# Optimization experiments

Hardware: AMD Instinct MI355X
Metric: run time of the kernel (lower is better)

The kernel has to match this reference:

```python
import jax, jax.numpy as jnp
import numpy as np

D_MODEL = 384
D_STATE = 16
D_CONV = 3
EXPAND = 2
D_INNER = EXPAND * D_MODEL          # 768
DT_RANK = (D_MODEL + 15) // 16      # 24 (mamba_ssm 'auto' rank = ceil(d_model/16))
B_, H_, W_ = 8, 32, 32


def setup_inputs() -> dict:
    key = jax.random.key(0)
    ks = jax.random.split(key, 8)
    s = lambda k, shape, scale: jax.random.normal(k, shape, jnp.float32) * scale
    x = jax.random.normal(ks[0], (B_, D_MODEL, H_, W_), jnp.float32)
    in_proj_w = s(ks[1], (2 * D_INNER, D_MODEL), 0.02)
    conv_w = s(ks[2], (D_INNER, D_CONV), 0.1)          # depthwise conv kernels
    conv_b = jnp.zeros((D_INNER,), jnp.float32)
    x_proj_w = s(ks[3], (DT_RANK + 2 * D_STATE, D_INNER), 0.02)
    dt_proj_w = s(ks[4], (D_INNER, DT_RANK), 0.1)
    # bias so that softplus(bias) ~= 0.01 (mamba dt init)
    dt_proj_b = jnp.log(jnp.expm1(jnp.full((D_INNER,), 0.01, jnp.float32)))
    # S4D-real init: A = -[1..N] per channel, stored as log
    A_log = jnp.log(jnp.broadcast_to(
        jnp.arange(1, D_STATE + 1, dtype=jnp.float32), (D_INNER, D_STATE)))
    D = jnp.ones((D_INNER,), jnp.float32)
    out_proj_w = s(ks[5], (D_MODEL, D_INNER), 0.02)
    return dict(x=x, in_proj_w=in_proj_w, conv_w=conv_w, conv_b=conv_b,
                x_proj_w=x_proj_w, dt_proj_w=dt_proj_w, dt_proj_b=dt_proj_b,
                A_log=A_log, D=D, out_proj_w=out_proj_w)


def _mamba(xseq, in_proj_w, conv_w, conv_b, x_proj_w,
           dt_proj_w, dt_proj_b, A_log, D, out_proj_w):
    # xseq: (B, L, d_model)
    B, L, _ = xseq.shape
    xz = xseq @ in_proj_w.T                         # (B, L, 2*d_inner)
    xin, z = jnp.split(xz, 2, axis=-1)

    # depthwise causal conv1d over L
    xc = jnp.transpose(xin, (0, 2, 1))              # (B, d_inner, L)
    xc = jnp.pad(xc, ((0, 0), (0, 0), (D_CONV - 1, 0)))
    xc = jax.lax.conv_general_dilated(
        xc, conv_w[:, None, :], (1,), 'VALID',
        dimension_numbers=('NCH', 'OIH', 'NCH'),
        feature_group_count=D_INNER)
    xc = xc + conv_b[None, :, None]
    u = jax.nn.silu(jnp.transpose(xc, (0, 2, 1)))   # (B, L, d_inner)

    dbc = u @ x_proj_w.T                            # (B, L, dt_rank + 2N)
    dt = dbc[..., :DT_RANK]
    Bm = dbc[..., DT_RANK:DT_RANK + D_STATE]        # (B, L, N)
    Cm = dbc[..., DT_RANK + D_STATE:]               # (B, L, N)
    dt = jax.nn.softplus(dt @ dt_proj_w.T + dt_proj_b)  # (B, L, d_inner)
    A = -jnp.exp(A_log)                             # (d_inner, N)

    def step(h, inp):
        dt_t, B_t, C_t, u_t = inp                   # (B,d), (B,N), (B,N), (B,d)
        dA = jnp.exp(dt_t[..., None] * A)           # (B, d_inner, N)
        h = dA * h + (dt_t * u_t)[..., None] * B_t[:, None, :]
        y = jnp.einsum('bdn,bn->bd', h, C_t)
        return h, y

    h0 = jnp.zeros((B, D_INNER, D_STATE), xseq.dtype)
    _, ys = jax.lax.scan(step, h0, (jnp.swapaxes(dt, 0, 1), jnp.swapaxes(Bm, 0, 1),
                                    jnp.swapaxes(Cm, 0, 1), jnp.swapaxes(u, 0, 1)))
    y = jnp.swapaxes(ys, 0, 1) + u * D              # (B, L, d_inner)
    y = y * jax.nn.silu(z)
    return y @ out_proj_w.T                         # (B, L, d_model)


def reference(x, in_proj_w, conv_w, conv_b, x_proj_w,
              dt_proj_w, dt_proj_b, A_log, D, out_proj_w):
    # x: (B, C, H, W) -> sequence (B, H*W, C) -> Mamba -> back to (B, C, H, W)
    B, C, H, W = x.shape
    xseq = jnp.transpose(x, (0, 2, 3, 1)).reshape(B, H * W, C)
    y = _mamba(xseq, in_proj_w, conv_w, conv_b, x_proj_w,
               dt_proj_w, dt_proj_b, A_log, D, out_proj_w)
    return jnp.transpose(y.reshape(B, H, W, C), (0, 3, 1, 2))
```

## Files before the change

kernel.cpp:

```cpp
#include <hip/hip_runtime.h>

#define D_MODEL 384
#define D_STATE 16
#define D_INNER 768
#define DT_RANK 24
#define NB 8
#define LSEQ 1024
#define NROWS (NB * LSEQ)
#define DBC_N 56
#define SEG 16
#define NSEG 64

typedef unsigned short u16;
typedef __attribute__((ext_vector_type(8))) short bf16x8;
typedef __attribute__((ext_vector_type(4))) float f32x4;
typedef __attribute__((ext_vector_type(16))) float f32x16;

__device__ __forceinline__ float silu(float x) { return x / (1.f + __expf(-x)); }

__device__ __forceinline__ u16 f2bf_rne(float v, float& hval) {
    unsigned u = __builtin_bit_cast(unsigned, v);
    unsigned h = (u + 0x7FFFu + ((u >> 16) & 1u)) >> 16;
    hval = __builtin_bit_cast(float, h << 16);
    return (u16)h;
}

__device__ __forceinline__ void split2(float v, u16& h, u16& l) {
    float hval, dummy;
    h = f2bf_rne(v, hval);
    l = f2bf_rne(v - hval, dummy);
}

template <int CTRL>
__device__ __forceinline__ float dpp_mov(float v) {
    return __builtin_bit_cast(float, __builtin_amdgcn_update_dpp(
        0, __builtin_bit_cast(int, v), CTRL, 0xf, 0xf, false));
}

__global__ __launch_bounds__(256) void k_splitw(const float* __restrict__ src,
                                                u16* __restrict__ hi, u16* __restrict__ lo,
                                                int count) {
    const int i = blockIdx.x * 256 + threadIdx.x;
    if (i >= count) return;
    u16 h, l;
    split2(src[i], h, l);
    hi[i] = h; lo[i] = l;
}

__global__ __launch_bounds__(256) void k_splitw_pad(const float* __restrict__ src,
                                                    u16* __restrict__ hi, u16* __restrict__ lo) {
    const int i = blockIdx.x * 256 + threadIdx.x;
    if (i >= 64 * 768) return;
    const int row = i / 768;
    u16 h = 0, l = 0;
    if (row < DBC_N) split2(src[i], h, l);
    hi[i] = h; lo[i] = l;
}

__global__ __launch_bounds__(256) void k_splitT(const float* __restrict__ src,
                                                u16* __restrict__ hi, u16* __restrict__ lo,
                                                int R) {
    __shared__ float s[32][33];
    const int r0 = blockIdx.x * 32, c0 = blockIdx.y * 32, b = blockIdx.z;
    const int t = threadIdx.x;
    const int cc = t & 31, rr = t >> 5;
#pragma unroll
    for (int p = 0; p < 4; ++p)
        s[rr + p * 8][cc] = src[((size_t)b * R + r0 + rr + p * 8) * LSEQ + c0 + cc];
    __syncthreads();
    const int rr2 = t & 31, cc2 = t >> 5;
#pragma unroll
    for (int p = 0; p < 4; ++p) {
        const int c = cc2 + p * 8;
        u16 h, l;
        split2(s[rr2][c], h, l);
        const size_t idx = ((size_t)b * LSEQ + c0 + c) * R + r0 + rr2;
        hi[idx] = h; lo[idx] = l;
    }
}

template <int K, int MODE>
__global__ __launch_bounds__(256) void k_gemm(const u16* __restrict__ Ahi,
                                              const u16* __restrict__ Alo,
                                              const u16* __restrict__ Bhi,
                                              const u16* __restrict__ Blo,
                                              float* __restrict__ out0,
                                              float* __restrict__ out1) {
    constexpr int KT = K / 32;
    __shared__ u16 lA[2][2][512 * 8];
    __shared__ u16 lB[2][2][512 * 8];
    const int tid = threadIdx.x;
    const int n0 = blockIdx.x * 128;
    const int m0 = blockIdx.y * 128;

    bf16x8 rah[2], ral[2], rbh[2], rbl[2];
    auto load_kt = [&](int kt) {
        const int ko = kt * 32;
#pragma unroll
        for (int i = 0; i < 2; ++i) {
            const int slot = tid + 256 * i;
            const size_t aoff = (size_t)(m0 + (slot & 127)) * K + ko + (slot >> 7) * 8;
            const size_t boff = (size_t)(n0 + (slot & 127)) * K + ko + (slot >> 7) * 8;
            rah[i] = *reinterpret_cast<const bf16x8*>(Ahi + aoff);
            ral[i] = *reinterpret_cast<const bf16x8*>(Alo + aoff);
            rbh[i] = *reinterpret_cast<const bf16x8*>(Bhi + boff);
            rbl[i] = *reinterpret_cast<const bf16x8*>(Blo + boff);
        }
    };
    auto write_kt = [&](int buf) {
#pragma unroll
        for (int i = 0; i < 2; ++i) {
            const int slot = tid + 256 * i;
            *reinterpret_cast<bf16x8*>(&lA[buf][0][slot * 8]) = rah[i];
            *reinterpret_cast<bf16x8*>(&lA[buf][1][slot * 8]) = ral[i];
            *reinterpret_cast<bf16x8*>(&lB[buf][0][slot * 8]) = rbh[i];
            *reinterpret_cast<bf16x8*>(&lB[buf][1][slot * 8]) = rbl[i];
        }
    };

    load_kt(0);
    write_kt(0);
    if (KT > 1) load_kt(1);

    const int lane = tid & 63, w = tid >> 6;
    const int wm = w >> 1, wn = w & 1;
    const int r32 = lane & 31, g2 = lane >> 5;

    f32x16 acc[2][2] = {};
    for (int kt = 0; kt < KT; ++kt) {
        const int cur = kt & 1;
        __syncthreads();
#pragma unroll
        for (int ks = 0; ks < 2; ++ks) {
            bf16x8 ah[2], al[2], bh[2], bl[2];
#pragma unroll
            for (int mi = 0; mi < 2; ++mi) {
                const int ai = ((ks * 2 + g2) * 128 + wm * 64 + mi * 32 + r32) * 8;
                ah[mi] = *reinterpret_cast<const bf16x8*>(&lA[cur][0][ai]);
                al[mi] = *reinterpret_cast<const bf16x8*>(&lA[cur][1][ai]);
            }
#pragma unroll
            for (int ni = 0; ni < 2; ++ni) {
                const int bi = ((ks * 2 + g2) * 128 + wn * 64 + ni * 32 + r32) * 8;
                bh[ni] = *reinterpret_cast<const bf16x8*>(&lB[cur][0][bi]);
                bl[ni] = *reinterpret_cast<const bf16x8*>(&lB[cur][1][bi]);
            }
#pragma unroll
            for (int mi = 0; mi < 2; ++mi)
#pragma unroll
                for (int ni = 0; ni < 2; ++ni) {
                    acc[mi][ni] = __builtin_amdgcn_mfma_f32_32x32x16_bf16(
                        ah[mi], bh[ni], acc[mi][ni], 0, 0, 0);
                    acc[mi][ni] = __builtin_amdgcn_mfma_f32_32x32x16_bf16(
                        ah[mi], bl[ni], acc[mi][ni], 0, 0, 0);
                    acc[mi][ni] = __builtin_amdgcn_mfma_f32_32x32x16_bf16(
                        al[mi], bh[ni], acc[mi][ni], 0, 0, 0);
                }
        }
        if (kt + 1 < KT) {
            __syncthreads();
            write_kt(cur ^ 1);
            if (kt + 2 < KT) load_kt(kt + 2);
        }
    }

    const int b_idx = m0 >> 10;
    const int l0b = m0 & 1023;
    if (MODE == 0) {
        if (n0 < D_INNER) {
#pragma unroll
            for (int mi = 0; mi < 2; ++mi) {
#pragma unroll
                for (int ni = 0; ni < 2; ++ni) {
                    const int n = n0 + wn * 64 + ni * 32 + r32;
#pragma unroll
                    for (int reg = 0; reg < 16; ++reg) {
                        const int m = m0 + wm * 64 + mi * 32 +
                                      (reg & 3) + 8 * (reg >> 2) + 4 * g2;
                        out0[(size_t)m * D_INNER + n] = acc[mi][ni][reg];
                    }
                }
            }
        } else {
#pragma unroll
            for (int mi = 0; mi < 2; ++mi) {
#pragma unroll
                for (int ni = 0; ni < 2; ++ni) {
                    const int d = (n0 - D_INNER) + wn * 64 + ni * 32 + r32;
#pragma unroll
                    for (int q = 0; q < 4; ++q) {
                        const int l = l0b + wm * 64 + mi * 32 + 8 * q + 4 * g2;
                        float4 v = make_float4(silu(acc[mi][ni][q * 4 + 0]),
                                               silu(acc[mi][ni][q * 4 + 1]),
                                               silu(acc[mi][ni][q * 4 + 2]),
                                               silu(acc[mi][ni][q * 4 + 3]));
                        *reinterpret_cast<float4*>(
                            &out1[((size_t)b_idx * D_INNER + d) * LSEQ + l]) = v;
                    }
                }
            }
        }
    } else {
#pragma unroll
        for (int mi = 0; mi < 2; ++mi) {
#pragma unroll
            for (int ni = 0; ni < 2; ++ni) {
                const int n = n0 + wn * 64 + ni * 32 + r32;
#pragma unroll
                for (int q = 0; q < 4; ++q) {
                    const int l = l0b + wm * 64 + mi * 32 + 8 * q + 4 * g2;
                    float4 v = make_float4(acc[mi][ni][q * 4 + 0], acc[mi][ni][q * 4 + 1],
                                           acc[mi][ni][q * 4 + 2], acc[mi][ni][q * 4 + 3]);
                    *reinterpret_cast<float4*>(
                        &out0[((size_t)b_idx * D_MODEL + n) * LSEQ + l]) = v;
                }
            }
        }
    }
}

__global__ __launch_bounds__(256) void k_xprojm(const u16* __restrict__ Uhi,
                                                const u16* __restrict__ Ulo,
                                                const u16* __restrict__ Whi,
                                                const u16* __restrict__ Wlo,
                                                float* __restrict__ dbc,
                                                float* __restrict__ bct) {
    __shared__ u16 lA[2][2][64 * 32];
    __shared__ u16 lB[2][2][64 * 32];
    const int tid = threadIdx.x;
    const int m0 = blockIdx.x * 64;
    const int arow = tid >> 2, acol = (tid & 3) * 8;

    bf16x8 rah, ral, rbh, rbl;
    auto load_kt = [&](int kt) {
        const int ko = kt * 32;
        const size_t aoff = (size_t)(m0 + arow) * D_INNER + ko + acol;
        const size_t boff = (size_t)arow * D_INNER + ko + acol;
        rah = *reinterpret_cast<const bf16x8*>(Uhi + aoff);
        ral = *reinterpret_cast<const bf16x8*>(Ulo + aoff);
        rbh = *reinterpret_cast<const bf16x8*>(Whi + boff);
        rbl = *reinterpret_cast<const bf16x8*>(Wlo + boff);
    };
    auto write_kt = [&](int buf) {
        *reinterpret_cast<bf16x8*>(&lA[buf][0][arow * 32 + acol]) = rah;
        *reinterpret_cast<bf16x8*>(&lA[buf][1][arow * 32 + acol]) = ral;
        *reinterpret_cast<bf16x8*>(&lB[buf][0][arow * 32 + acol]) = rbh;
        *reinterpret_cast<bf16x8*>(&lB[buf][1][arow * 32 + acol]) = rbl;
    };

    load_kt(0);
    write_kt(0);
    load_kt(1);

    const int lane = tid & 63, w = tid >> 6;
    const int fr = lane & 15, g = lane >> 4;
    f32x4 acc[4] = {};
    for (int kt = 0; kt < 24; ++kt) {
        const int cur = kt & 1;
        __syncthreads();
        const int af = (w * 16 + fr) * 32 + g * 8;
        bf16x8 ah = *reinterpret_cast<const bf16x8*>(&lA[cur][0][af]);
        bf16x8 al = *reinterpret_cast<const bf16x8*>(&lA[cur][1][af]);
        bf16x8 bh[4], bl[4];
#pragma unroll
        for (int ni = 0; ni < 4; ++ni) {
            const int bf = (ni * 16 + fr) * 32 + g * 8;
            bh[ni] = *reinterpret_cast<const bf16x8*>(&lB[cur][0][bf]);
            bl[ni] = *reinterpret_cast<const bf16x8*>(&lB[cur][1][bf]);
        }
#pragma unroll
        for (int ni = 0; ni < 4; ++ni) {
            acc[ni] = __builtin_amdgcn_mfma_f32_16x16x32_bf16(ah, bh[ni], acc[ni], 0, 0, 0);
            acc[ni] = __builtin_amdgcn_mfma_f32_16x16x32_bf16(ah, bl[ni], acc[ni], 0, 0, 0);
            acc[ni] = __builtin_amdgcn_mfma_f32_16x16x32_bf16(al, bh[ni], acc[ni], 0, 0, 0);
        }
        if (kt + 1 < 24) {
            __syncthreads();
            write_kt(cur ^ 1);
            if (kt + 2 < 24) load_kt(kt + 2);
        }
    }

    const int b_idx = m0 >> 10;
#pragma unroll
    for (int ni = 0; ni < 4; ++ni) {
        const int col = ni * 16 + fr;
#pragma unroll
        for (int j = 0; j < 4; ++j) {
            const int r = w * 16 + g * 4 + j;
            const float v = acc[ni][j];
            if (col < DT_RANK) {
                dbc[(size_t)(m0 + r) * DBC_N + col] = v;
            } else if (col < DBC_N) {
                bct[((size_t)b_idx * 32 + (col - DT_RANK)) * LSEQ + ((m0 & 1023) + r)] = v;
            }
        }
    }
}

__global__ __launch_bounds__(256) void k_conv(const float* __restrict__ xin,
                                              const float* __restrict__ cw,
                                              const float* __restrict__ cb,
                                              u16* __restrict__ u_hi,
                                              u16* __restrict__ u_lo,
                                              float* __restrict__ uT) {
    __shared__ float xs[34][32];
    __shared__ float us[32][33];
    const int d0 = blockIdx.x * 32;
    const int l0 = blockIdx.y * 32;
    const int b  = blockIdx.z;
    const int t = threadIdx.x;
    const int dd = t & 31, r = t >> 5;
    for (int rr = r; rr < 34; rr += 8) {
        const int l = l0 - 2 + rr;
        xs[rr][dd] = (l >= 0) ? xin[((size_t)b * LSEQ + l) * D_INNER + d0 + dd] : 0.f;
    }
    __syncthreads();
    const float w0 = cw[(d0 + dd) * 3 + 0], w1 = cw[(d0 + dd) * 3 + 1], w2 = cw[(d0 + dd) * 3 + 2];
    const float bv = cb[d0 + dd];
#pragma unroll
    for (int p = 0; p < 4; ++p) {
        const int li = r + p * 8;
        float acc = bv;
        acc = fmaf(xs[li + 0][dd], w0, acc);
        acc = fmaf(xs[li + 1][dd], w1, acc);
        acc = fmaf(xs[li + 2][dd], w2, acc);
        const float uv = silu(acc);
        u16 h, l;
        split2(uv, h, l);
        const size_t idx = ((size_t)b * LSEQ + l0 + li) * D_INNER + d0 + dd;
        u_hi[idx] = h; u_lo[idx] = l;
        us[li][dd] = uv;
    }
    __syncthreads();
    const int ll = t & 31, dg = t >> 5;
#pragma unroll
    for (int p = 0; p < 4; ++p) {
        const int dl = dg + p * 8;
        uT[((size_t)b * D_INNER + d0 + dl) * LSEQ + l0 + ll] = us[ll][dl];
    }
}

__global__ __launch_bounds__(256) void k_dtproj(const float* __restrict__ dbc,
                                                const float* __restrict__ W,
                                                const float* __restrict__ bias,
                                                float* __restrict__ dtT) {
    __shared__ float sd[64][25];
    __shared__ float sw[64][24];
    __shared__ float sb[64];
    const int d0 = blockIdx.x * 64;
    const int row0 = blockIdx.y * 64;
    const int b = row0 >> 10, lr0 = row0 & 1023;
    const int t = threadIdx.x;
    for (int e = t; e < 64 * 24; e += 256) {
        const int rl = e / 24, rr = e - rl * 24;
        sd[rl][rr] = dbc[(size_t)(row0 + rl) * DBC_N + rr];
        sw[rl][rr] = W[(size_t)(d0 + rl) * DT_RANK + rr];
    }
    if (t < 64) sb[t] = bias[d0 + t];
    __syncthreads();
    const int ll = t & 63, dg = t >> 6;
    for (int dd = 0; dd < 16; ++dd) {
        const int dl = dg * 16 + dd;
        float acc = sb[dl];
#pragma unroll
        for (int r = 0; r < DT_RANK; ++r) acc = fmaf(sd[ll][r], sw[dl][r], acc);
        const float v = (acc > 20.f) ? acc : log1pf(__expf(acc));
        dtT[((size_t)b * D_INNER + d0 + dl) * LSEQ + lr0 + ll] = v;
    }
}

__global__ __launch_bounds__(1024, 8) void k_scan(float* dtyT,
                                                  const float* __restrict__ uT,
                                                  const float* __restrict__ szT,
                                                  const float* __restrict__ bct,
                                                  const float* __restrict__ A_log,
                                                  const float* __restrict__ Dp) {
    __shared__ float dt_s[LSEQ], u_s[LSEQ], sz_s[LSEQ], y_s[LSEQ];
    __shared__ float Pb[16][NSEG + 2], Hb[16][NSEG + 2];
    const int t = threadIdx.x;
    const int d = blockIdx.x;
    const int b = blockIdx.y;
    const size_t base = ((size_t)b * D_INNER + d) * LSEQ;
    if (t < 256) {
        *reinterpret_cast<float4*>(&dt_s[t * 4]) =
            *reinterpret_cast<const float4*>(&dtyT[base + t * 4]);
    } else if (t < 512) {
        const int q = (t - 256) * 4;
        *reinterpret_cast<float4*>(&u_s[q]) = *reinterpret_cast<const float4*>(&uT[base + q]);
    } else if (t < 768) {
        const int q = (t - 512) * 4;
        *reinterpret_cast<float4*>(&sz_s[q]) = *reinterpret_cast<const float4*>(&szT[base + q]);
    }
    const int n = t & 15, seg = t >> 4;
    const float Aval2 = -__expf(A_log[d * D_STATE + n]) * 1.44269504088896f;
    const float Dv = Dp[d];
    float Breg[SEG];
    {
        const size_t bb = ((size_t)b * 32 + n) * LSEQ + seg * SEG;
#pragma unroll
        for (int q = 0; q < SEG; q += 4)
            *reinterpret_cast<float4*>(&Breg[q]) = *reinterpret_cast<const float4*>(&bct[bb + q]);
    }
    __syncthreads();
    const int l0 = seg * SEG;
    float h = 0.f, P = 1.f;
#pragma unroll
    for (int l = 0; l < SEG; ++l) {
        const float dtv = dt_s[l0 + l];
        const float a = exp2f(dtv * Aval2);
        const float x = dtv * u_s[l0 + l] * Breg[l];
        Breg[l] = x;
        h = fmaf(a, h, x);
        P *= a;
    }
    Pb[n][seg] = P;
    Hb[n][seg] = h;
    float Creg[SEG];
    {
        const size_t cc = ((size_t)b * 32 + 16 + n) * LSEQ + seg * SEG;
#pragma unroll
        for (int q = 0; q < SEG; q += 4)
            *reinterpret_cast<float4*>(&Creg[q]) = *reinterpret_cast<const float4*>(&bct[cc + q]);
    }
    __syncthreads();
    {
        const int w = t >> 6, lane = t & 63;
        float Pw = Pb[w][lane], Hw = Hb[w][lane];
#pragma unroll
        for (int off = 1; off < NSEG; off <<= 1) {
            const float Pp = __shfl_up(Pw, off);
            const float Hp = __shfl_up(Hw, off);
            if (lane >= off) {
                Hw = fmaf(Hp, Pw, Hw);
                Pw *= Pp;
            }
        }
        Hb[w][lane] = Hw;
    }
    __syncthreads();
    h = (seg == 0) ? 0.f : Hb[n][seg - 1];
#pragma unroll
    for (int l = 0; l < SEG; ++l) {
        const float a = exp2f(dt_s[l0 + l] * Aval2);
        h = fmaf(a, h, Breg[l]);
        float p = h * Creg[l];
        p += dpp_mov<0x128>(p);
        p += dpp_mov<0x124>(p);
        p += dpp_mov<0x122>(p);
        p += dpp_mov<0x121>(p);
        if (n == 0) {
            const float u_v = u_s[l0 + l];
            y_s[l0 + l] = fmaf(u_v, Dv, p) * sz_s[l0 + l];
        }
    }
    __syncthreads();
    if (t < 256)
        *reinterpret_cast<float4*>(&dtyT[base + t * 4]) =
            *reinterpret_cast<const float4*>(&y_s[t * 4]);
}

extern "C" void kernel_launch(void* const* d_in, const int* in_sizes, int n_in,
                              void* d_out, int out_size, void* d_ws, size_t ws_size,
                              hipStream_t stream) {
    const float* x         = (const float*)d_in[0];
    const float* in_proj_w = (const float*)d_in[1];
    const float* conv_w    = (const float*)d_in[2];
    const float* conv_b    = (const float*)d_in[3];
    const float* x_proj_w  = (const float*)d_in[4];
    const float* dt_proj_w = (const float*)d_in[5];
    const float* dt_proj_b = (const float*)d_in[6];
    const float* A_log     = (const float*)d_in[7];
    const float* Dp        = (const float*)d_in[8];
    const float* out_proj_w= (const float*)d_in[9];
    float* out = (float*)d_out;

    const size_t SB = (size_t)NROWS * D_INNER * 4;
    char* wsb = (char*)d_ws;
    float* xin   = (float*)(wsb);
    float* szT   = (float*)(wsb + SB);
    u16*  u_hi   = (u16*)  (wsb + 2 * SB);
    u16*  u_lo   = u_hi + (size_t)NROWS * D_INNER;
    float* uT    = (float*)(wsb + 3 * SB);
    float* dbc   = (float*)(wsb + 4 * SB);
    float* bct   = (float*)(wsb + 4 * SB + 1835008);
    u16*  Wi_hi  = (u16*) (wsb + 4 * SB + 1835008 + 1048576);
    u16*  Wi_lo  = Wi_hi + 1536 * 384;
    u16*  Wo_hi  = Wi_lo + 1536 * 384;
    u16*  Wo_lo  = Wo_hi + 384 * 768;
    u16*  Wx_hi  = Wo_lo + 384 * 768;
    u16*  Wx_lo  = Wx_hi + 64 * 768;
    u16*  Ax_hi  = (u16*)uT;
    u16*  Ax_lo  = Ax_hi + (size_t)NROWS * 384;
    u16*  Ay_hi  = (u16*)uT;
    u16*  Ay_lo  = Ay_hi + (size_t)NROWS * 768;
    float* dtyT  = xin;

    k_splitw<<<(1536 * 384 + 255) / 256, 256, 0, stream>>>(in_proj_w, Wi_hi, Wi_lo, 1536 * 384);
    k_splitw<<<(384 * 768 + 255) / 256, 256, 0, stream>>>(out_proj_w, Wo_hi, Wo_lo, 384 * 768);
    k_splitw_pad<<<(64 * 768 + 255) / 256, 256, 0, stream>>>(x_proj_w, Wx_hi, Wx_lo);
    k_splitT<<<dim3(12, 32, NB), 256, 0, stream>>>(x, Ax_hi, Ax_lo, 384);
    k_gemm<384, 0><<<dim3(12, 64), 256, 0, stream>>>(Ax_hi, Ax_lo, Wi_hi, Wi_lo, xin, szT);
    k_conv<<<dim3(24, 32, NB), 256, 0, stream>>>(xin, conv_w, conv_b, u_hi, u_lo, uT);
    k_xprojm<<<NROWS / 64, 256, 0, stream>>>(u_hi, u_lo, Wx_hi, Wx_lo, dbc, bct);
    k_dtproj<<<dim3(12, NROWS / 64), 256, 0, stream>>>(dbc, dt_proj_w, dt_proj_b, dtyT);
    k_scan<<<dim3(D_INNER, NB), 1024, 0, stream>>>(dtyT, uT, szT, bct, A_log, Dp);
    k_splitT<<<dim3(24, 32, NB), 256, 0, stream>>>(dtyT, Ay_hi, Ay_lo, 768);
    k_gemm<768, 1><<<dim3(3, 64), 256, 0, stream>>>(Ay_hi, Ay_lo, Wo_hi, Wo_lo, out, nullptr);
}
```

Measured before the change: 289.3 us.

## Fuse dt projection into scan and use transpose-reduce for output sums

Removes the separate dt-projection kernel and computes softplus(dt) inside the scan kernel: each of the 1024 threads computes one timestep's dt from the dbc row and the per-channel weights. This avoids writing and re-reading the transposed dt tensor. The 16-lane C·h reduction is also replaced with a butterfly transpose-reduce over DPP, so every thread ends up with one output timestep and writes it directly, with no shared y/sz staging. The cost is that the dbc rows are re-read once for each of the 768 channels (cache-dependent), and each thread now holds more registers.

```diff
diff --git a/kernel.cpp b/kernel.cpp
--- a/kernel.cpp
+++ b/kernel.cpp
@@ -35,6 +35,9 @@
 __device__ __forceinline__ float dpp_mov(float v) {
     return __builtin_bit_cast(float, __builtin_amdgcn_update_dpp(
         0, __builtin_bit_cast(int, v), CTRL, 0xf, 0xf, false));
+}
+__device__ __forceinline__ float dpp_xor4(float v) {
+    return dpp_mov<0x141>(dpp_mov<0x1B>(v));
 }
 
 __global__ __launch_bounds__(256) void k_splitw(const float* __restrict__ src,
@@ -341,58 +344,57 @@
     }
 }
 
-__global__ __launch_bounds__(256) void k_dtproj(const float* __restrict__ dbc,
-                                                const float* __restrict__ W,
-                                                const float* __restrict__ bias,
-                                                float* __restrict__ dtT) {
-    __shared__ float sd[64][25];
-    __shared__ float sw[64][24];
-    __shared__ float sb[64];
-    const int d0 = blockIdx.x * 64;
-    const int row0 = blockIdx.y * 64;
-    const int b = row0 >> 10, lr0 = row0 & 1023;
-    const int t = threadIdx.x;
-    for (int e = t; e < 64 * 24; e += 256) {
-        const int rl = e / 24, rr = e - rl * 24;
-        sd[rl][rr] = dbc[(size_t)(row0 + rl) * DBC_N + rr];
-        sw[rl][rr] = W[(size_t)(d0 + rl) * DT_RANK + rr];
-    }
-    if (t < 64) sb[t] = bias[d0 + t];
-    __syncthreads();
-    const int ll = t & 63, dg = t >> 6;
-    for (int dd = 0; dd < 16; ++dd) {
-        const int dl = dg * 16 + dd;
-        float acc = sb[dl];
-#pragma unroll
-        for (int r = 0; r < DT_RANK; ++r) acc = fmaf(sd[ll][r], sw[dl][r], acc);
-        const float v = (acc > 20.f) ? acc : log1pf(__expf(acc));
-        dtT[((size_t)b * D_INNER + d0 + dl) * LSEQ + lr0 + ll] = v;
-    }
-}
-
-__global__ __launch_bounds__(1024, 8) void k_scan(float* dtyT,
+__global__ __launch_bounds__(1024, 8) void k_scan(float* __restrict__ yT,
                                                   const float* __restrict__ uT,
                                                   const float* __restrict__ szT,
                                                   const float* __restrict__ bct,
+                                                  const float* __restrict__ dbc,
+                                                  const float* __restrict__ Wdt,
+                                                  const float* __restrict__ bdt,
                                                   const float* __restrict__ A_log,
                                                   const float* __restrict__ Dp) {
-    __shared__ float dt_s[LSEQ], u_s[LSEQ], sz_s[LSEQ], y_s[LSEQ];
+    __shared__ float dt_s[LSEQ], u_s[LSEQ];
     __shared__ float Pb[16][NSEG + 2], Hb[16][NSEG + 2];
     const int t = threadIdx.x;
     const int d = blockIdx.x;
     const int b = blockIdx.y;
     const size_t base = ((size_t)b * D_INNER + d) * LSEQ;
-    if (t < 256) {
-        *reinterpret_cast<float4*>(&dt_s[t * 4]) =
-            *reinterpret_cast<const float4*>(&dtyT[base + t * 4]);
-    } else if (t < 512) {
-        const int q = (t - 256) * 4;
-        *reinterpret_cast<float4*>(&u_s[q]) = *reinterpret_cast<const float4*>(&uT[base + q]);
-    } else if (t < 768) {
-        const int q = (t - 512) * 4;
-        *reinterpret_cast<float4*>(&sz_s[q]) = *reinterpret_cast<const float4*>(&szT[base + q]);
-    }
     const int n = t & 15, seg = t >> 4;
+
+    if (t < 256)
+        *reinterpret_cast<float4*>(&u_s[t * 4]) =
+            *reinterpret_cast<const float4*>(&uT[base + t * 4]);
+
+    {
+        const float4 w0 = *reinterpret_cast<const float4*>(&Wdt[d * DT_RANK + 0]);
+        const float4 w1 = *reinterpret_cast<const float4*>(&Wdt[d * DT_RANK + 4]);
+        const float4 w2 = *reinterpret_cast<const float4*>(&Wdt[d * DT_RANK + 8]);
+        const float4 w3 = *reinterpret_cast<const float4*>(&Wdt[d * DT_RANK + 12]);
+        const float4 w4 = *reinterpret_cast<const float4*>(&Wdt[d * DT_RANK + 16]);
+        const float4 w5 = *reinterpret_cast<const float4*>(&Wdt[d * DT_RANK + 20]);
+        const float* dr = &dbc[(size_t)((b << 10) + t) * DBC_N];
+        const float4 v0 = *reinterpret_cast<const float4*>(dr + 0);
+        const float4 v1 = *reinterpret_cast<const float4*>(dr + 4);
+        const float4 v2 = *reinterpret_cast<const float4*>(dr + 8);
+        const float4 v3 = *reinterpret_cast<const float4*>(dr + 12);
+        const float4 v4 = *reinterpret_cast<const float4*>(dr + 16);
+        const float4 v5 = *reinterpret_cast<const float4*>(dr + 20);
+        float acc = bdt[d];
+        acc = fmaf(v0.x, w0.x, acc); acc = fmaf(v0.y, w0.y, acc);
+        acc = fmaf(v0.z, w0.z, acc); acc = fmaf(v0.w, w0.w, acc);
+        acc = fmaf(v1.x, w1.x, acc); acc = fmaf(v1.y, w1.y, acc);
+        acc = fmaf(v1.z, w1.z, acc); acc = fmaf(v1.w, w1.w, acc);
+        acc = fmaf(v2.x, w2.x, acc); acc = fmaf(v2.y, w2.y, acc);
+        acc = fmaf(v2.z, w2.z, acc); acc = fmaf(v2.w, w2.w, acc);
+        acc = fmaf(v3.x, w3.x, acc); acc = fmaf(v3.y, w3.y, acc);
+        acc = fmaf(v3.z, w3.z, acc); acc = fmaf(v3.w, w3.w, acc);
+        acc = fmaf(v4.x, w4.x, acc); acc = fmaf(v4.y, w4.y, acc);
+        acc = fmaf(v4.z, w4.z, acc); acc = fmaf(v4.w, w4.w, acc);
+        acc = fmaf(v5.x, w5.x, acc); acc = fmaf(v5.y, w5.y, acc);
+        acc = fmaf(v5.z, w5.z, acc); acc = fmaf(v5.w, w5.w, acc);
+        dt_s[t] = (acc > 20.f) ? acc : log1pf(__expf(acc));
+    }
+
     const float Aval2 = -__expf(A_log[d * D_STATE + n]) * 1.44269504088896f;
     const float Dv = Dp[d];
     float Breg[SEG];
@@ -409,8 +411,9 @@
     for (int l = 0; l < SEG; ++l) {
         const float dtv = dt_s[l0 + l];
         const float a = exp2f(dtv * Aval2);
-        const float x = dtv * u_s[l0 + l] * Breg[l];
+        float x = dtv * u_s[l0 + l] * Breg[l];
         Breg[l] = x;
+        asm volatile("" : "+v"(Breg[l]));
         h = fmaf(a, h, x);
         P *= a;
     }
@@ -422,6 +425,8 @@
 #pragma unroll
         for (int q = 0; q < SEG; q += 4)
             *reinterpret_cast<float4*>(&Creg[q]) = *reinterpret_cast<const float4*>(&bct[cc + q]);
+#pragma unroll
+        for (int l = 0; l < SEG; ++l) asm volatile("" : "+v"(Creg[l]));
     }
     __syncthreads();
     {
@@ -439,25 +444,49 @@
         Hb[w][lane] = Hw;
     }
     __syncthreads();
-    h = (seg == 0) ? 0.f : Hb[n][seg - 1];
+    float y[SEG];
+    float hh = (seg == 0) ? 0.f : Hb[n][seg - 1];
 #pragma unroll
     for (int l = 0; l < SEG; ++l) {
         const float a = exp2f(dt_s[l0 + l] * Aval2);
-        h = fmaf(a, h, Breg[l]);
-        float p = h * Creg[l];
-        p += dpp_mov<0x128>(p);
-        p += dpp_mov<0x124>(p);
-        p += dpp_mov<0x122>(p);
-        p += dpp_mov<0x121>(p);
-        if (n == 0) {
-            const float u_v = u_s[l0 + l];
-            y_s[l0 + l] = fmaf(u_v, Dv, p) * sz_s[l0 + l];
-        }
-    }
-    __syncthreads();
-    if (t < 256)
-        *reinterpret_cast<float4*>(&dtyT[base + t * 4]) =
-            *reinterpret_cast<const float4*>(&y_s[t * 4]);
+        hh = fmaf(a, hh, Breg[l]);
+        y[l] = hh * Creg[l];
+        asm volatile("" : "+v"(y[l]));
+    }
+    float Y;
+    {
+        float z[8];
+        const bool h8 = (n & 8) != 0;
+#pragma unroll
+        for (int j = 0; j < 8; ++j) {
+            const float give = h8 ? y[j] : y[j + 8];
+            const float keep = h8 ? y[j + 8] : y[j];
+            z[j] = keep + dpp_mov<0x128>(give);
+        }
+        float z2[4];
+        const bool h4 = (n & 4) != 0;
+#pragma unroll
+        for (int j = 0; j < 4; ++j) {
+            const float give = h4 ? z[j] : z[j + 4];
+            const float keep = h4 ? z[j + 4] : z[j];
+            z2[j] = keep + dpp_xor4(give);
+        }
+        float z3[2];
+        const bool h2 = (n & 2) != 0;
+#pragma unroll
+        for (int j = 0; j < 2; ++j) {
+            const float give = h2 ? z2[j] : z2[j + 2];
+            const float keep = h2 ? z2[j + 2] : z2[j];
+            z3[j] = keep + dpp_mov<0x4E>(give);
+        }
+        const bool h1 = (n & 1) != 0;
+        const float give = h1 ? z3[0] : z3[1];
+        const float keep = h1 ? z3[1] : z3[0];
+        Y = keep + dpp_mov<0xB1>(give);
+    }
+    const float u_v = u_s[t];
+    const float sz = szT[base + t];
+    yT[base + t] = fmaf(u_v, Dv, Y) * sz;
 }
 
 extern "C" void kernel_launch(void* const* d_in, const int* in_sizes, int n_in,
@@ -494,7 +523,7 @@
     u16*  Ax_lo  = Ax_hi + (size_t)NROWS * 384;
     u16*  Ay_hi  = (u16*)uT;
     u16*  Ay_lo  = Ay_hi + (size_t)NROWS * 768;
-    float* dtyT  = xin;
+    float* yT    = xin;
 
     k_splitw<<<(1536 * 384 + 255) / 256, 256, 0, stream>>>(in_proj_w, Wi_hi, Wi_lo, 1536 * 384);
     k_splitw<<<(384 * 768 + 255) / 256, 256, 0, stream>>>(out_proj_w, Wo_hi, Wo_lo, 384 * 768);
@@ -503,8 +532,8 @@
     k_gemm<384, 0><<<dim3(12, 64), 256, 0, stream>>>(Ax_hi, Ax_lo, Wi_hi, Wi_lo, xin, szT);
     k_conv<<<dim3(24, 32, NB), 256, 0, stream>>>(xin, conv_w, conv_b, u_hi, u_lo, uT);
     k_xprojm<<<NROWS / 64, 256, 0, stream>>>(u_hi, u_lo, Wx_hi, Wx_lo, dbc, bct);
-    k_dtproj<<<dim3(12, NROWS / 64), 256, 0, stream>>>(dbc, dt_proj_w, dt_proj_b, dtyT);
-    k_scan<<<dim3(D_INNER, NB), 1024, 0, stream>>>(dtyT, uT, szT, bct, A_log, Dp);
-    k_splitT<<<dim3(24, 32, NB), 256, 0, stream>>>(dtyT, Ay_hi, Ay_lo, 768);
+    k_scan<<<dim3(D_INNER, NB), 1024, 0, stream>>>(yT, uT, szT, bct, dbc,
+                                                   dt_proj_w, dt_proj_b, A_log, Dp);
+    k_splitT<<<dim3(24, 32, NB), 256, 0, stream>>>(yT, Ay_hi, Ay_lo, 768);
     k_gemm<768, 1><<<dim3(3, 64), 256, 0, stream>>>(Ay_hi, Ay_lo, Wo_hi, Wo_lo, out, nullptr);
 }
```

After: 298.0 us. 1.03x slower.
